# Optimization experiments

Hardware: AMD Instinct MI355X
Metric: run time of the kernel (lower is better)

## Reference

```python
import jax, jax.numpy as jnp
import numpy as np

DIM = 256
HEADS = 8
HEAD_DIM = DIM // HEADS
SCALE = HEAD_DIM ** -0.5
B, N = 2048, 49
NW = 64


def setup_inputs() -> dict:
    key = jax.random.key(0)
    ks = jax.random.split(key, 7)
    x = jax.random.normal(ks[0], (B, N, DIM), dtype=jnp.float32)
    mask = jax.random.normal(ks[1], (NW, N + 1, N + 1), dtype=jnp.float32)
    class_token = 0.02 * jax.random.normal(ks[2], (1, 1, DIM), dtype=jnp.float32)
    qkv_w = jax.random.normal(ks[3], (DIM, 3 * DIM), dtype=jnp.float32) / np.sqrt(DIM)
    qkv_b = jnp.zeros((3 * DIM,), dtype=jnp.float32)
    proj_w = jax.random.normal(ks[4], (DIM, DIM), dtype=jnp.float32) / np.sqrt(DIM)
    proj_b = jnp.zeros((DIM,), dtype=jnp.float32)
    return {"x": x, "mask": mask, "class_token": class_token,
            "qkv_w": qkv_w, "qkv_b": qkv_b, "proj_w": proj_w, "proj_b": proj_b}


def reference(x, mask, class_token, qkv_w, qkv_b, proj_w, proj_b):
    b, n, c = x.shape
    n1 = n + 1
    # prepend learnable class token
    cls = jnp.broadcast_to(class_token, (b, 1, c))
    xc = jnp.concatenate([cls, x], axis=1)  # (B, N+1, C)
    # fused qkv projection
    qkv = xc @ qkv_w + qkv_b                 # (B, N+1, 3C)
    qkv = qkv.reshape(b, n1, 3, HEADS, HEAD_DIM)
    qkv = jnp.transpose(qkv, (2, 0, 3, 1, 4))  # (3, B, H, N+1, Dh)
    q, k, v = qkv[0] * SCALE, qkv[1], qkv[2]
    attn = jnp.einsum('bhid,bhjd->bhij', q, k)  # (B, H, N+1, N+1)
    # per-window additive mask bias
    nw = mask.shape[0]
    attn = attn.reshape(b // nw, nw, HEADS, n1, n1) + mask[None, :, None]
    attn = attn.reshape(b, HEADS, n1, n1)
    attn = jax.nn.softmax(attn, axis=-1)
    out = jnp.einsum('bhij,bhjd->bhid', attn, v)      # (B, H, N+1, Dh)
    out = jnp.transpose(out, (0, 2, 1, 3)).reshape(b, n1, c)
    out = out @ proj_w + proj_b
    return out[:, 0], out[:, 1:]
```

## Files before the change

### kernel.cpp

```cpp
#include <hip/hip_runtime.h>

#define NB    2048
#define N1    50
#define DIMC  256
#define NHEAD 8

typedef short  s16x8 __attribute__((ext_vector_type(8)));
typedef short  s16x4 __attribute__((ext_vector_type(4)));
typedef float  f32x4 __attribute__((ext_vector_type(4)));
typedef float  f32x2 __attribute__((ext_vector_type(2)));

__device__ __forceinline__ unsigned short f2bf(float f) {
    unsigned int u = __builtin_bit_cast(unsigned int, f);
    u = (u + 0x7FFFu + ((u >> 16) & 1u)) >> 16;
    return (unsigned short)u;
}
__device__ __forceinline__ s16x8 ld8(const unsigned short* p) {
    return *(const s16x8*)p;
}

__global__ void prep_kernel(const float* __restrict__ qkv_w, const float* __restrict__ proj_w,
                            const float* __restrict__ mask,
                            unsigned short* __restrict__ wqkvB, unsigned short* __restrict__ wprojB,
                            float* __restrict__ maskP) {
    int idx = blockIdx.x * 256 + threadIdx.x;
    {
        int wv = idx >> 12, q = (idx >> 6) & 63, k = idx & 63;
        float v = (k < 50) ? ((q < 50) ? mask[(wv * 50 + q) * 50 + k] : 0.f) : -1e30f;
        maskP[idx] = v;
    }
    if (idx < 196608) {
        int ks = idx / 24576, rem = idx - ks * 24576, n = rem >> 5, kk = rem & 31;
        wqkvB[idx] = f2bf(qkv_w[(ks * 32 + kk) * 768 + n]);
    }
    if (idx < 65536) {
        int ks = idx >> 13, rem = idx & 8191, n = rem >> 5, kk = rem & 31;
        wprojB[idx] = f2bf(proj_w[(ks * 32 + kk) * 256 + n]);
    }
}

__global__ __launch_bounds__(1024, 4) void fused_kernel(
        const float* __restrict__ x, const float* __restrict__ cls,
        const float* __restrict__ qkv_b, const unsigned short* __restrict__ wqkvB,
        const unsigned short* __restrict__ wprojB, const float* __restrict__ proj_b,
        const float* __restrict__ maskP, float* __restrict__ out) {
    __shared__ __align__(16) char smem_raw[152576];
    unsigned short* S   = (unsigned short*)smem_raw;
    unsigned short* sXC = S;
    unsigned short* sQ  = S + 16896;
    unsigned short* sK  = S + 37376;
    unsigned short* sVT = S + 57856;

    const int b = blockIdx.x, tid = threadIdx.x;
    const int lane = tid & 63, w = tid >> 6;
    const int ln15 = lane & 15, quad = lane >> 4, q8 = quad * 8;
    const int win = b & 63;
    const float SCALE = 0.17677669529663687f;

    #pragma unroll
    for (int i = 0; i < 8; ++i) {
        int p = i * 1024 + tid;
        int r = p >> 7, c = (p & 127) * 2;
        float v0, v1;
        if (r == 0)       { v0 = cls[c]; v1 = cls[c + 1]; }
        else if (r <= 49) { const float* px = &x[((size_t)b * 49 + (r - 1)) * 256 + c];
                            f32x2 t = *(const f32x2*)px; v0 = t[0]; v1 = t[1]; }
        else              { v0 = 0.f; v1 = 0.f; }
        *(unsigned int*)&sXC[r * 264 + c] = (unsigned int)f2bf(v0) | ((unsigned int)f2bf(v1) << 16);
    }
    s16x8 bcur[3];
    #pragma unroll
    for (int nt = 0; nt < 3; ++nt)
        bcur[nt] = ld8(wqkvB + (w * 48 + nt * 16 + ln15) * 32 + q8);
    __syncthreads();

    f32x4 acc[4][3];
    #pragma unroll
    for (int mt = 0; mt < 4; ++mt)
        #pragma unroll
        for (int nt = 0; nt < 3; ++nt) acc[mt][nt] = f32x4{0.f, 0.f, 0.f, 0.f};

    #pragma unroll
    for (int ks = 0; ks < 8; ++ks) {
        s16x8 bnext[3];
        if (ks < 7) {
            const unsigned short* src = wqkvB + (ks + 1) * 24576;
            #pragma unroll
            for (int nt = 0; nt < 3; ++nt)
                bnext[nt] = ld8(src + (w * 48 + nt * 16 + ln15) * 32 + q8);
        }
        s16x8 af[4];
        #pragma unroll
        for (int mt = 0; mt < 4; ++mt)
            af[mt] = ld8(&sXC[(mt * 16 + ln15) * 264 + ks * 32 + q8]);
        #pragma unroll
        for (int mt = 0; mt < 4; ++mt)
            #pragma unroll
            for (int nt = 0; nt < 3; ++nt)
                acc[mt][nt] = __builtin_amdgcn_mfma_f32_16x16x32_bf16(af[mt], bcur[nt], acc[mt][nt], 0, 0, 0);
        if (ks < 7) {
            #pragma unroll
            for (int nt = 0; nt < 3; ++nt) bcur[nt] = bnext[nt];
        }
    }

    #pragma unroll
    for (int nt = 0; nt < 3; ++nt) {
        const int gc = w * 48 + nt * 16 + ln15;
        const int type = (w * 48 + nt * 16) >> 8;
        const int hd = (gc >> 5) & 7, dd = gc & 31;
        const float bias = qkv_b[gc];
        if (type == 0) {
            #pragma unroll
            for (int mt = 0; mt < 4; ++mt)
                #pragma unroll
                for (int i = 0; i < 4; ++i)
                    sQ[hd * 2560 + (mt * 16 + quad * 4 + i) * 40 + dd] = f2bf((acc[mt][nt][i] + bias) * SCALE);
        } else if (type == 1) {
            #pragma unroll
            for (int mt = 0; mt < 4; ++mt)
                #pragma unroll
                for (int i = 0; i < 4; ++i)
                    sK[hd * 2560 + (mt * 16 + quad * 4 + i) * 40 + dd] = f2bf(acc[mt][nt][i] + bias);
        } else {
            #pragma unroll
            for (int mt = 0; mt < 4; ++mt) {
                s16x4 pk;
                #pragma unroll
                for (int i = 0; i < 4; ++i) pk[i] = f2bf(acc[mt][nt][i] + bias);
                *(s16x4*)&sVT[hd * 2304 + dd * 72 + mt * 16 + quad * 4] = pk;
            }
        }
    }
    __syncthreads();

    {
        const int h = w >> 1, rh = w & 1, qt0 = rh * 2;
        unsigned short* sPw = sQ + h * 2560 + rh * 1280;

        s16x8 ak[4];
        #pragma unroll
        for (int kt = 0; kt < 4; ++kt)
            ak[kt] = ld8(&sK[h * 2560 + (kt * 16 + ln15) * 40 + q8]);

        f32x4 st[2][4];
        #pragma unroll
        for (int mt = 0; mt < 2; ++mt) {
            s16x8 bq = ld8(&sQ[h * 2560 + ((qt0 + mt) * 16 + ln15) * 40 + q8]);
            #pragma unroll
            for (int kt = 0; kt < 4; ++kt) {
                f32x4 z = {0.f, 0.f, 0.f, 0.f};
                st[mt][kt] = __builtin_amdgcn_mfma_f32_16x16x32_bf16(ak[kt], bq, z, 0, 0, 0);
            }
        }
        s16x8 pb[2][2];
        #pragma unroll
        for (int mt = 0; mt < 2; ++mt) {
            float sum = 0.f;
            #pragma unroll
            for (int kt = 0; kt < 4; ++kt) {
                f32x4 mk = *(const f32x4*)&maskP[((size_t)(win * 64 + (qt0 + mt) * 16 + ln15)) * 64 + kt * 16 + quad * 4];
                #pragma unroll
                for (int i = 0; i < 4; ++i) {
                    float e = __expf(st[mt][kt][i] + mk[i]);
                    st[mt][kt][i] = e;
                    sum += e;
                }
            }
            sum += __shfl_xor(sum, 16, 64);
            sum += __shfl_xor(sum, 32, 64);
            const float inv = 1.f / sum;
            #pragma unroll
            for (int kt = 0; kt < 4; ++kt) {
                s16x4 pk;
                #pragma unroll
                for (int i = 0; i < 4; ++i) pk[i] = f2bf(st[mt][kt][i] * inv);
                *(s16x4*)&sPw[ln15 * 72 + kt * 16 + quad * 4] = pk;
            }
            asm volatile("s_waitcnt lgkmcnt(0)" ::: "memory");
            pb[mt][0] = ld8(&sPw[ln15 * 72 + q8]);
            pb[mt][1] = ld8(&sPw[ln15 * 72 + 32 + q8]);
        }
        s16x8 av[2][2];
        #pragma unroll
        for (int dt = 0; dt < 2; ++dt)
            #pragma unroll
            for (int kk = 0; kk < 2; ++kk)
                av[dt][kk] = ld8(&sVT[h * 2304 + (dt * 16 + ln15) * 72 + kk * 32 + q8]);
        f32x4 o[2][2];
        #pragma unroll
        for (int mt = 0; mt < 2; ++mt)
            #pragma unroll
            for (int dt = 0; dt < 2; ++dt) o[mt][dt] = f32x4{0.f, 0.f, 0.f, 0.f};
        #pragma unroll
        for (int mt = 0; mt < 2; ++mt)
            #pragma unroll
            for (int dt = 0; dt < 2; ++dt)
                #pragma unroll
                for (int kk = 0; kk < 2; ++kk)
                    o[mt][dt] = __builtin_amdgcn_mfma_f32_16x16x32_bf16(av[dt][kk], pb[mt][kk], o[mt][dt], 0, 0, 0);
        #pragma unroll
        for (int mt = 0; mt < 2; ++mt) {
            const int qg = (qt0 + mt) * 16 + ln15;
            #pragma unroll
            for (int dt = 0; dt < 2; ++dt) {
                s16x4 pk;
                #pragma unroll
                for (int i = 0; i < 4; ++i) pk[i] = f2bf(o[mt][dt][i]);
                *(s16x4*)&sXC[qg * 264 + h * 32 + dt * 16 + quad * 4] = pk;
            }
        }
    }
    __syncthreads();

    {
        const int wm3 = w >> 3, wn3 = w & 7;
        s16x8 b3[2];
        #pragma unroll
        for (int nt = 0; nt < 2; ++nt)
            b3[nt] = ld8(wprojB + (wn3 * 32 + nt * 16 + ln15) * 32 + q8);
        f32x4 a3[2][2];
        #pragma unroll
        for (int mt = 0; mt < 2; ++mt)
            #pragma unroll
            for (int nt = 0; nt < 2; ++nt) a3[mt][nt] = f32x4{0.f, 0.f, 0.f, 0.f};
        #pragma unroll
        for (int ks = 0; ks < 8; ++ks) {
            s16x8 b3n[2];
            if (ks < 7) {
                const unsigned short* src = wprojB + (ks + 1) * 8192;
                #pragma unroll
                for (int nt = 0; nt < 2; ++nt)
                    b3n[nt] = ld8(src + (wn3 * 32 + nt * 16 + ln15) * 32 + q8);
            }
            s16x8 af3[2];
            #pragma unroll
            for (int mt = 0; mt < 2; ++mt)
                af3[mt] = ld8(&sXC[(wm3 * 32 + mt * 16 + ln15) * 264 + ks * 32 + q8]);
            #pragma unroll
            for (int mt = 0; mt < 2; ++mt)
                #pragma unroll
                for (int nt = 0; nt < 2; ++nt)
                    a3[mt][nt] = __builtin_amdgcn_mfma_f32_16x16x32_bf16(af3[mt], b3[nt], a3[mt][nt], 0, 0, 0);
            if (ks < 7) {
                #pragma unroll
                for (int nt = 0; nt < 2; ++nt) b3[nt] = b3n[nt];
            }
        }
        #pragma unroll
        for (int nt = 0; nt < 2; ++nt) {
            const int gc = wn3 * 32 + nt * 16 + ln15;
            const float bias = proj_b[gc];
            #pragma unroll
            for (int mt = 0; mt < 2; ++mt) {
                #pragma unroll
                for (int i = 0; i < 4; ++i) {
                    const int t = wm3 * 32 + mt * 16 + quad * 4 + i;
                    const float v = a3[mt][nt][i] + bias;
                    if (t == 0)      out[(size_t)b * 256 + gc] = v;
                    else if (t < 50) out[(size_t)524288 + ((size_t)b * 49 + (t - 1)) * 256 + gc] = v;
                }
            }
        }
    }
}

extern "C" void kernel_launch(void* const* d_in, const int* in_sizes, int n_in,
                              void* d_out, int out_size, void* d_ws, size_t ws_size,
                              hipStream_t stream) {
    const float* x      = (const float*)d_in[0];
    const float* mask   = (const float*)d_in[1];
    const float* cls    = (const float*)d_in[2];
    const float* qkv_w  = (const float*)d_in[3];
    const float* qkv_b  = (const float*)d_in[4];
    const float* proj_w = (const float*)d_in[5];
    const float* proj_b = (const float*)d_in[6];
    float* out = (float*)d_out;

    unsigned short* wqkvB  = (unsigned short*)d_ws;
    unsigned short* wprojB = (unsigned short*)((char*)d_ws + 393216);
    float*          maskP  = (float*)((char*)d_ws + 524288);

    prep_kernel<<<1024, 256, 0, stream>>>(qkv_w, proj_w, mask, wqkvB, wprojB, maskP);
    fused_kernel<<<NB, 1024, 0, stream>>>(x, cls, qkv_b, wqkvB, wprojB, proj_b, maskP, out);
}
```

Measured before the change: 312.0 us.

## Vectorize global I/O and repartition QKV columns so epilogue writes are packed

Loads x with 16-byte per-lane vectors, one row per wave, instead of 8-byte strided chunks. Each wave is now assigned the matching 16-column slice of Q, K and V. The MFMA operands for Q/K and for the output projection are swapped so each lane holds four consecutive columns, which allows packed 8-byte LDS stores and 16-byte global output stores in place of scalar ones. The proj weight prefetch is hoisted before the barrier. This relies on the transposed accumulator layout being indexed correctly in every epilogue.

```diff
diff --git a/kernel.cpp b/kernel.cpp
--- a/kernel.cpp
+++ b/kernel.cpp
@@ -9,6 +9,7 @@
 typedef short  s16x4 __attribute__((ext_vector_type(4)));
 typedef float  f32x4 __attribute__((ext_vector_type(4)));
 typedef float  f32x2 __attribute__((ext_vector_type(2)));
+typedef unsigned int u32x2 __attribute__((ext_vector_type(2)));
 
 __device__ __forceinline__ unsigned short f2bf(float f) {
     unsigned int u = __builtin_bit_cast(unsigned int, f);
@@ -58,20 +59,21 @@
     const float SCALE = 0.17677669529663687f;
 
     #pragma unroll
-    for (int i = 0; i < 8; ++i) {
-        int p = i * 1024 + tid;
-        int r = p >> 7, c = (p & 127) * 2;
-        float v0, v1;
-        if (r == 0)       { v0 = cls[c]; v1 = cls[c + 1]; }
-        else if (r <= 49) { const float* px = &x[((size_t)b * 49 + (r - 1)) * 256 + c];
-                            f32x2 t = *(const f32x2*)px; v0 = t[0]; v1 = t[1]; }
-        else              { v0 = 0.f; v1 = 0.f; }
-        *(unsigned int*)&sXC[r * 264 + c] = (unsigned int)f2bf(v0) | ((unsigned int)f2bf(v1) << 16);
+    for (int it = 0; it < 4; ++it) {
+        const int r = it * 16 + w;
+        f32x4 t;
+        if (r == 0)       t = *(const f32x4*)&cls[lane * 4];
+        else if (r <= 49) t = *(const f32x4*)&x[((size_t)b * 49 + (r - 1)) * 256 + lane * 4];
+        else              t = f32x4{0.f, 0.f, 0.f, 0.f};
+        u32x2 wv;
+        wv[0] = (unsigned int)f2bf(t[0]) | ((unsigned int)f2bf(t[1]) << 16);
+        wv[1] = (unsigned int)f2bf(t[2]) | ((unsigned int)f2bf(t[3]) << 16);
+        *(u32x2*)&sXC[r * 264 + lane * 4] = wv;
     }
     s16x8 bcur[3];
     #pragma unroll
     for (int nt = 0; nt < 3; ++nt)
-        bcur[nt] = ld8(wqkvB + (w * 48 + nt * 16 + ln15) * 32 + q8);
+        bcur[nt] = ld8(wqkvB + (nt * 256 + w * 16 + ln15) * 32 + q8);
     __syncthreads();
 
     f32x4 acc[4][3];
@@ -87,49 +89,42 @@
             const unsigned short* src = wqkvB + (ks + 1) * 24576;
             #pragma unroll
             for (int nt = 0; nt < 3; ++nt)
-                bnext[nt] = ld8(src + (w * 48 + nt * 16 + ln15) * 32 + q8);
+                bnext[nt] = ld8(src + (nt * 256 + w * 16 + ln15) * 32 + q8);
         }
         s16x8 af[4];
         #pragma unroll
         for (int mt = 0; mt < 4; ++mt)
             af[mt] = ld8(&sXC[(mt * 16 + ln15) * 264 + ks * 32 + q8]);
         #pragma unroll
-        for (int mt = 0; mt < 4; ++mt)
-            #pragma unroll
-            for (int nt = 0; nt < 3; ++nt)
-                acc[mt][nt] = __builtin_amdgcn_mfma_f32_16x16x32_bf16(af[mt], bcur[nt], acc[mt][nt], 0, 0, 0);
+        for (int mt = 0; mt < 4; ++mt) {
+            acc[mt][0] = __builtin_amdgcn_mfma_f32_16x16x32_bf16(bcur[0], af[mt], acc[mt][0], 0, 0, 0);
+            acc[mt][1] = __builtin_amdgcn_mfma_f32_16x16x32_bf16(bcur[1], af[mt], acc[mt][1], 0, 0, 0);
+            acc[mt][2] = __builtin_amdgcn_mfma_f32_16x16x32_bf16(af[mt], bcur[2], acc[mt][2], 0, 0, 0);
+        }
         if (ks < 7) {
             #pragma unroll
             for (int nt = 0; nt < 3; ++nt) bcur[nt] = bnext[nt];
         }
     }
 
-    #pragma unroll
-    for (int nt = 0; nt < 3; ++nt) {
-        const int gc = w * 48 + nt * 16 + ln15;
-        const int type = (w * 48 + nt * 16) >> 8;
-        const int hd = (gc >> 5) & 7, dd = gc & 31;
-        const float bias = qkv_b[gc];
-        if (type == 0) {
-            #pragma unroll
-            for (int mt = 0; mt < 4; ++mt)
-                #pragma unroll
-                for (int i = 0; i < 4; ++i)
-                    sQ[hd * 2560 + (mt * 16 + quad * 4 + i) * 40 + dd] = f2bf((acc[mt][nt][i] + bias) * SCALE);
-        } else if (type == 1) {
-            #pragma unroll
-            for (int mt = 0; mt < 4; ++mt)
-                #pragma unroll
-                for (int i = 0; i < 4; ++i)
-                    sK[hd * 2560 + (mt * 16 + quad * 4 + i) * 40 + dd] = f2bf(acc[mt][nt][i] + bias);
-        } else {
-            #pragma unroll
-            for (int mt = 0; mt < 4; ++mt) {
-                s16x4 pk;
-                #pragma unroll
-                for (int i = 0; i < 4; ++i) pk[i] = f2bf(acc[mt][nt][i] + bias);
-                *(s16x4*)&sVT[hd * 2304 + dd * 72 + mt * 16 + quad * 4] = pk;
-            }
+    {
+        const int hd = w >> 1, ddb = (w & 1) * 16;
+        const f32x4 bq4 = *(const f32x4*)&qkv_b[w * 16 + quad * 4];
+        const f32x4 bk4 = *(const f32x4*)&qkv_b[256 + w * 16 + quad * 4];
+        const float bv  = qkv_b[512 + w * 16 + ln15];
+        #pragma unroll
+        for (int mt = 0; mt < 4; ++mt) {
+            const int row = (mt * 16 + ln15) * 40 + ddb + quad * 4;
+            s16x4 wq, wk, wv;
+            #pragma unroll
+            for (int i = 0; i < 4; ++i) {
+                wq[i] = f2bf((acc[mt][0][i] + bq4[i]) * SCALE);
+                wk[i] = f2bf(acc[mt][1][i] + bk4[i]);
+                wv[i] = f2bf(acc[mt][2][i] + bv);
+            }
+            *(s16x4*)&sQ[hd * 2560 + row] = wq;
+            *(s16x4*)&sK[hd * 2560 + row] = wk;
+            *(s16x4*)&sVT[hd * 2304 + (ddb + ln15) * 72 + mt * 16 + quad * 4] = wv;
         }
     }
     __syncthreads();
@@ -204,21 +199,21 @@
             const int qg = (qt0 + mt) * 16 + ln15;
             #pragma unroll
             for (int dt = 0; dt < 2; ++dt) {
-                s16x4 pk;
-                #pragma unroll
-                for (int i = 0; i < 4; ++i) pk[i] = f2bf(o[mt][dt][i]);
-                *(s16x4*)&sXC[qg * 264 + h * 32 + dt * 16 + quad * 4] = pk;
-            }
-        }
-    }
+                s16x4 ov;
+                #pragma unroll
+                for (int i = 0; i < 4; ++i) ov[i] = f2bf(o[mt][dt][i]);
+                *(s16x4*)&sXC[qg * 264 + h * 32 + dt * 16 + quad * 4] = ov;
+            }
+        }
+    }
+    const int wm3 = w >> 3, wn3 = w & 7;
+    s16x8 b3[2];
+    #pragma unroll
+    for (int nt = 0; nt < 2; ++nt)
+        b3[nt] = ld8(wprojB + (wn3 * 32 + nt * 16 + ln15) * 32 + q8);
     __syncthreads();
 
     {
-        const int wm3 = w >> 3, wn3 = w & 7;
-        s16x8 b3[2];
-        #pragma unroll
-        for (int nt = 0; nt < 2; ++nt)
-            b3[nt] = ld8(wprojB + (wn3 * 32 + nt * 16 + ln15) * 32 + q8);
         f32x4 a3[2][2];
         #pragma unroll
         for (int mt = 0; mt < 2; ++mt)
@@ -241,7 +236,7 @@
             for (int mt = 0; mt < 2; ++mt)
                 #pragma unroll
                 for (int nt = 0; nt < 2; ++nt)
-                    a3[mt][nt] = __builtin_amdgcn_mfma_f32_16x16x32_bf16(af3[mt], b3[nt], a3[mt][nt], 0, 0, 0);
+                    a3[mt][nt] = __builtin_amdgcn_mfma_f32_16x16x32_bf16(b3[nt], af3[mt], a3[mt][nt], 0, 0, 0);
             if (ks < 7) {
                 #pragma unroll
                 for (int nt = 0; nt < 2; ++nt) b3[nt] = b3n[nt];
@@ -249,17 +244,16 @@
         }
         #pragma unroll
         for (int nt = 0; nt < 2; ++nt) {
-            const int gc = wn3 * 32 + nt * 16 + ln15;
-            const float bias = proj_b[gc];
+            const int cb = wn3 * 32 + nt * 16 + quad * 4;
+            const f32x4 b4 = *(const f32x4*)&proj_b[cb];
             #pragma unroll
             for (int mt = 0; mt < 2; ++mt) {
-                #pragma unroll
-                for (int i = 0; i < 4; ++i) {
-                    const int t = wm3 * 32 + mt * 16 + quad * 4 + i;
-                    const float v = a3[mt][nt][i] + bias;
-                    if (t == 0)      out[(size_t)b * 256 + gc] = v;
-                    else if (t < 50) out[(size_t)524288 + ((size_t)b * 49 + (t - 1)) * 256 + gc] = v;
-                }
+                const int t = wm3 * 32 + mt * 16 + ln15;
+                f32x4 v;
+                #pragma unroll
+                for (int i = 0; i < 4; ++i) v[i] = a3[mt][nt][i] + b4[i];
+                if (t == 0)      *(f32x4*)&out[(size_t)b * 256 + cb] = v;
+                else if (t < 50) *(f32x4*)&out[524288 + ((size_t)b * 49 + (t - 1)) * 256 + cb] = v;
             }
         }
     }
```

Measured after the change: 303.9 us. 1.03x faster.

## Split fused attention into per-half-head QKV+attention kernel and separate projection kernel

Applied to the files above, without the earlier changes.

Replaces the single 1024-thread fused kernel with two launches. The first computes QKV and attention for half of the heads per block, using 4096 blocks with smaller shared memory to raise occupancy. It writes the bf16 attention output to a workspace buffer. The second kernel does the output projection, which adds a global round trip of about 64 MB and re-reads x once per head half. The fused path is kept as a fallback when the workspace is too small.

```diff
diff --git a/kernel.cpp b/kernel.cpp
--- a/kernel.cpp
+++ b/kernel.cpp
@@ -36,6 +36,255 @@
     if (idx < 65536) {
         int ks = idx >> 13, rem = idx & 8191, n = rem >> 5, kk = rem & 31;
         wprojB[idx] = f2bf(proj_w[(ks * 32 + kk) * 256 + n]);
+    }
+}
+
+__global__ __launch_bounds__(512, 6) void qkvattn_kernel(
+        const float* __restrict__ x, const float* __restrict__ cls,
+        const float* __restrict__ qkv_b, const unsigned short* __restrict__ wqkvB,
+        const float* __restrict__ maskP, unsigned short* __restrict__ og) {
+    __shared__ __align__(16) char smem_raw[54272];
+    unsigned short* S   = (unsigned short*)smem_raw;
+    unsigned short* sXC = S;
+    unsigned short* sQ  = S;
+    unsigned short* sK  = S + 9216;
+    unsigned short* sVT = S + 18432;
+
+    const int p = blockIdx.x, tid = threadIdx.x;
+    const int lane = tid & 63, w = tid >> 6;
+    const int ln15 = lane & 15, quad = lane >> 4, q8 = quad * 8;
+    const int b  = ((p >> 4) << 3) | (p & 7);
+    const int hh = ((p >> 3) & 1) << 2;
+    const int win = b & 63;
+    const float SCALE = 0.17677669529663687f;
+
+    #pragma unroll
+    for (int i = 0; i < 16; ++i) {
+        int pp = i * 512 + tid;
+        int r = pp >> 7, c = (pp & 127) * 2;
+        float v0, v1;
+        if (r == 0)       { v0 = cls[c]; v1 = cls[c + 1]; }
+        else if (r <= 49) { const float* px = &x[((size_t)b * 49 + (r - 1)) * 256 + c];
+                            f32x2 t = *(const f32x2*)px; v0 = t[0]; v1 = t[1]; }
+        else              { v0 = 0.f; v1 = 0.f; }
+        *(unsigned int*)&sXC[r * 264 + c] = (unsigned int)f2bf(v0) | ((unsigned int)f2bf(v1) << 16);
+    }
+    s16x8 bcur[3];
+    int g0[3];
+    #pragma unroll
+    for (int nt = 0; nt < 3; ++nt) {
+        const int sc0 = w * 48 + nt * 16;
+        const int seg = sc0 >> 7;
+        g0[nt] = seg * 256 + hh * 32 + (sc0 & 127);
+        bcur[nt] = ld8(wqkvB + (g0[nt] + ln15) * 32 + q8);
+    }
+    __syncthreads();
+
+    f32x4 acc[4][3];
+    #pragma unroll
+    for (int mt = 0; mt < 4; ++mt)
+        #pragma unroll
+        for (int nt = 0; nt < 3; ++nt) acc[mt][nt] = f32x4{0.f, 0.f, 0.f, 0.f};
+
+    #pragma unroll
+    for (int ks = 0; ks < 8; ++ks) {
+        s16x8 bnext[3];
+        if (ks < 7) {
+            const unsigned short* src = wqkvB + (ks + 1) * 24576;
+            #pragma unroll
+            for (int nt = 0; nt < 3; ++nt)
+                bnext[nt] = ld8(src + (g0[nt] + ln15) * 32 + q8);
+        }
+        s16x8 af[4];
+        #pragma unroll
+        for (int mt = 0; mt < 4; ++mt)
+            af[mt] = ld8(&sXC[(mt * 16 + ln15) * 264 + ks * 32 + q8]);
+        #pragma unroll
+        for (int mt = 0; mt < 4; ++mt)
+            #pragma unroll
+            for (int nt = 0; nt < 3; ++nt)
+                acc[mt][nt] = __builtin_amdgcn_mfma_f32_16x16x32_bf16(af[mt], bcur[nt], acc[mt][nt], 0, 0, 0);
+        if (ks < 7) {
+            #pragma unroll
+            for (int nt = 0; nt < 3; ++nt) bcur[nt] = bnext[nt];
+        }
+    }
+    __syncthreads();
+
+    #pragma unroll
+    for (int nt = 0; nt < 3; ++nt) {
+        const int sc0 = w * 48 + nt * 16;
+        const int seg = sc0 >> 7;
+        const int gcl = (sc0 & 127) + ln15;
+        const int hd = gcl >> 5, dd = gcl & 31;
+        const float bias = qkv_b[seg * 256 + hh * 32 + gcl];
+        if (seg == 0) {
+            #pragma unroll
+            for (int mt = 0; mt < 4; ++mt)
+                #pragma unroll
+                for (int i = 0; i < 4; ++i)
+                    sQ[hd * 2304 + (mt * 16 + quad * 4 + i) * 36 + dd] = f2bf((acc[mt][nt][i] + bias) * SCALE);
+        } else if (seg == 1) {
+            #pragma unroll
+            for (int mt = 0; mt < 4; ++mt)
+                #pragma unroll
+                for (int i = 0; i < 4; ++i)
+                    sK[hd * 2304 + (mt * 16 + quad * 4 + i) * 36 + dd] = f2bf(acc[mt][nt][i] + bias);
+        } else {
+            #pragma unroll
+            for (int mt = 0; mt < 4; ++mt) {
+                s16x4 pk;
+                #pragma unroll
+                for (int i = 0; i < 4; ++i) pk[i] = f2bf(acc[mt][nt][i] + bias);
+                *(s16x4*)&sVT[(hd * 32 + dd) * 68 + mt * 16 + quad * 4] = pk;
+            }
+        }
+    }
+    __syncthreads();
+
+    {
+        const int h = w >> 1, rh = w & 1, qt0 = rh * 2;
+        unsigned short* sPw = sQ + h * 2304 + rh * 1152;
+
+        s16x8 ak[4];
+        #pragma unroll
+        for (int kt = 0; kt < 4; ++kt)
+            ak[kt] = ld8(&sK[h * 2304 + (kt * 16 + ln15) * 36 + q8]);
+
+        f32x4 st[2][4];
+        #pragma unroll
+        for (int mt = 0; mt < 2; ++mt) {
+            s16x8 bq = ld8(&sQ[h * 2304 + ((qt0 + mt) * 16 + ln15) * 36 + q8]);
+            #pragma unroll
+            for (int kt = 0; kt < 4; ++kt) {
+                f32x4 z = {0.f, 0.f, 0.f, 0.f};
+                st[mt][kt] = __builtin_amdgcn_mfma_f32_16x16x32_bf16(ak[kt], bq, z, 0, 0, 0);
+            }
+        }
+        s16x8 pb[2][2];
+        #pragma unroll
+        for (int mt = 0; mt < 2; ++mt) {
+            float sum = 0.f;
+            #pragma unroll
+            for (int kt = 0; kt < 4; ++kt) {
+                f32x4 mk = *(const f32x4*)&maskP[((size_t)(win * 64 + (qt0 + mt) * 16 + ln15)) * 64 + kt * 16 + quad * 4];
+                #pragma unroll
+                for (int i = 0; i < 4; ++i) {
+                    float e = __expf(st[mt][kt][i] + mk[i]);
+                    st[mt][kt][i] = e;
+                    sum += e;
+                }
+            }
+            sum += __shfl_xor(sum, 16, 64);
+            sum += __shfl_xor(sum, 32, 64);
+            const float inv = 1.f / sum;
+            #pragma unroll
+            for (int kt = 0; kt < 4; ++kt) {
+                s16x4 pk;
+                #pragma unroll
+                for (int i = 0; i < 4; ++i) pk[i] = f2bf(st[mt][kt][i] * inv);
+                *(s16x4*)&sPw[ln15 * 72 + kt * 16 + quad * 4] = pk;
+            }
+            asm volatile("s_waitcnt lgkmcnt(0)" ::: "memory");
+            pb[mt][0] = ld8(&sPw[ln15 * 72 + q8]);
+            pb[mt][1] = ld8(&sPw[ln15 * 72 + 32 + q8]);
+        }
+        s16x8 av[2][2];
+        #pragma unroll
+        for (int dt = 0; dt < 2; ++dt)
+            #pragma unroll
+            for (int kk = 0; kk < 2; ++kk)
+                av[dt][kk] = ld8(&sVT[(h * 32 + dt * 16 + ln15) * 68 + kk * 32 + q8]);
+        f32x4 o[2][2];
+        #pragma unroll
+        for (int mt = 0; mt < 2; ++mt)
+            #pragma unroll
+            for (int dt = 0; dt < 2; ++dt) o[mt][dt] = f32x4{0.f, 0.f, 0.f, 0.f};
+        #pragma unroll
+        for (int mt = 0; mt < 2; ++mt)
+            #pragma unroll
+            for (int dt = 0; dt < 2; ++dt)
+                #pragma unroll
+                for (int kk = 0; kk < 2; ++kk)
+                    o[mt][dt] = __builtin_amdgcn_mfma_f32_16x16x32_bf16(av[dt][kk], pb[mt][kk], o[mt][dt], 0, 0, 0);
+        #pragma unroll
+        for (int mt = 0; mt < 2; ++mt) {
+            const int qg = (qt0 + mt) * 16 + ln15;
+            #pragma unroll
+            for (int dt = 0; dt < 2; ++dt) {
+                s16x4 pk;
+                #pragma unroll
+                for (int i = 0; i < 4; ++i) pk[i] = f2bf(o[mt][dt][i]);
+                *(s16x4*)&og[((size_t)b * 64 + qg) * 256 + (hh + h) * 32 + dt * 16 + quad * 4] = pk;
+            }
+        }
+    }
+}
+
+__global__ __launch_bounds__(512, 6) void proj_kernel(
+        const unsigned short* __restrict__ og, const unsigned short* __restrict__ wprojB,
+        const float* __restrict__ proj_b, float* __restrict__ out) {
+    __shared__ __align__(16) unsigned short sO[64 * 264];
+
+    const int b = blockIdx.x, tid = threadIdx.x;
+    const int lane = tid & 63, w = tid >> 6;
+    const int ln15 = lane & 15, quad = lane >> 4, q8 = quad * 8;
+
+    #pragma unroll
+    for (int i = 0; i < 4; ++i) {
+        int idx = i * 512 + tid;
+        int r = idx >> 5, c8 = (idx & 31) * 8;
+        s16x8 v = ld8(og + ((size_t)b * 64 + r) * 256 + c8);
+        *(s16x8*)&sO[r * 264 + c8] = v;
+    }
+    s16x8 b3[2];
+    #pragma unroll
+    for (int nt = 0; nt < 2; ++nt)
+        b3[nt] = ld8(wprojB + (w * 32 + nt * 16 + ln15) * 32 + q8);
+    __syncthreads();
+
+    f32x4 a3[4][2];
+    #pragma unroll
+    for (int mt = 0; mt < 4; ++mt)
+        #pragma unroll
+        for (int nt = 0; nt < 2; ++nt) a3[mt][nt] = f32x4{0.f, 0.f, 0.f, 0.f};
+    #pragma unroll
+    for (int ks = 0; ks < 8; ++ks) {
+        s16x8 b3n[2];
+        if (ks < 7) {
+            const unsigned short* src = wprojB + (ks + 1) * 8192;
+            #pragma unroll
+            for (int nt = 0; nt < 2; ++nt)
+                b3n[nt] = ld8(src + (w * 32 + nt * 16 + ln15) * 32 + q8);
+        }
+        s16x8 af3[4];
+        #pragma unroll
+        for (int mt = 0; mt < 4; ++mt)
+            af3[mt] = ld8(&sO[(mt * 16 + ln15) * 264 + ks * 32 + q8]);
+        #pragma unroll
+        for (int mt = 0; mt < 4; ++mt)
+            #pragma unroll
+            for (int nt = 0; nt < 2; ++nt)
+                a3[mt][nt] = __builtin_amdgcn_mfma_f32_16x16x32_bf16(af3[mt], b3[nt], a3[mt][nt], 0, 0, 0);
+        if (ks < 7) {
+            #pragma unroll
+            for (int nt = 0; nt < 2; ++nt) b3[nt] = b3n[nt];
+        }
+    }
+    #pragma unroll
+    for (int nt = 0; nt < 2; ++nt) {
+        const int gc = w * 32 + nt * 16 + ln15;
+        const float bias = proj_b[gc];
+        #pragma unroll
+        for (int mt = 0; mt < 4; ++mt) {
+            #pragma unroll
+            for (int i = 0; i < 4; ++i) {
+                const int t = mt * 16 + quad * 4 + i;
+                const float v = a3[mt][nt][i] + bias;
+                if (t == 0)      out[(size_t)b * 256 + gc] = v;
+                else if (t < 50) out[(size_t)524288 + ((size_t)b * 49 + (t - 1)) * 256 + gc] = v;
+            }
+        }
     }
 }
 
@@ -280,7 +529,13 @@
     unsigned short* wqkvB  = (unsigned short*)d_ws;
     unsigned short* wprojB = (unsigned short*)((char*)d_ws + 393216);
     float*          maskP  = (float*)((char*)d_ws + 524288);
+    unsigned short* og     = (unsigned short*)((char*)d_ws + 1572864);
 
     prep_kernel<<<1024, 256, 0, stream>>>(qkv_w, proj_w, mask, wqkvB, wprojB, maskP);
-    fused_kernel<<<NB, 1024, 0, stream>>>(x, cls, qkv_b, wqkvB, wprojB, proj_b, maskP, out);
-}
+    if (ws_size >= (size_t)1572864 + 67108864) {
+        qkvattn_kernel<<<4096, 512, 0, stream>>>(x, cls, qkv_b, wqkvB, maskP, og);
+        proj_kernel<<<2048, 512, 0, stream>>>(og, wprojB, proj_b, out);
+    } else {
+        fused_kernel<<<NB, 1024, 0, stream>>>(x, cls, qkv_b, wqkvB, wprojB, proj_b, maskP, out);
+    }
+}
```

Measured after the change: 411.6 us. +31.9%, slower.
